# Kernel tuning notes

Measured on AMD Instinct MI355X. Metric: run time of the kernel, lower is better.

The kernel has to match this reference:

```python
import jax, jax.numpy as jnp
import numpy as np

N = 50000   # nodes
E = 800000  # edges
H = 4       # num_heads
D = 32      # out_dim
IN = 256    # in_dim


def setup_inputs() -> dict:
    key = jax.random.key(0)
    k0, k1, k2, k3, k4, k5 = jax.random.split(key, 6)
    h = jax.random.normal(k0, (N, IN), dtype=jnp.float32)
    # fl weight (torch Linear stores [out, in]), xavier-ish scale
    Wl = jax.random.normal(k1, (H * D, IN), dtype=jnp.float32) * (1.0 / np.sqrt(IN))
    # fc / fq are initialized to small constants in torch; use small random here
    fc = jax.random.normal(k2, (IN, H * D), dtype=jnp.float32) * 0.02
    fq = jax.random.normal(k3, (IN, H * D), dtype=jnp.float32) * 0.02
    src = jax.random.randint(k4, (E,), 0, N)
    dst = jax.random.randint(k5, (E,), 0, N)
    return {"h": h, "Wl": Wl, "fc": fc, "fq": fq, "src": src, "dst": dst}


def reference(h, Wl, fc, fq, src, dst):
    n = h.shape[0]
    ft = (h @ Wl.T).reshape(n, H, D)      # [N,H,D]
    ft_c = (h @ fc).reshape(n, H, D)      # [N,H,D]
    ft_q = (h @ fq).reshape(n, H, D)      # [N,H,D]

    # edge attention: c = ft_c[dst], q = ft_q[src] - c, a = ELU(sum(q*c))
    c = ft_c[dst]                         # [E,H,D]
    a = jax.nn.elu(jnp.sum((ft_q[src] - c) * c, axis=-1))  # [E,H]

    # segmented (per-destination) softmax over incoming edges, per head
    m = jax.ops.segment_max(a, dst, num_segments=n)        # [N,H]
    ex = jnp.exp(a - m[dst])
    s = jax.ops.segment_sum(ex, dst, num_segments=n)       # [N,H]
    attn = ex / s[dst]                                     # [E,H]

    # global top-k (smallest l_s) threshold + mass redistribution, per head
    l_s = int(0.713 * attn.shape[0])
    srt = jnp.sort(attn, axis=0)                           # ascending per head
    thd = srt[l_s - 1]                                     # [H] l_s-th smallest
    topk_sum = jnp.sum(srt[:l_s], axis=0)                  # [H]
    a2 = jnp.where(attn - thd < 0, jnp.zeros((), attn.dtype), attn)
    ratio = (jnp.sum(a2, axis=0) + topk_sum) / jnp.sum(a2, axis=0)  # [H]
    a3 = a2 * ratio                                        # [E,H]

    # weighted scatter-sum of source features to destinations
    out = jax.ops.segment_sum(ft[src] * a3[:, :, None], dst, num_segments=n)  # [N,H,D]

    # concat=True: cat(flattened heads, mean over heads of ft)
    return jnp.concatenate([out.reshape(n, -1), ft.mean(axis=1)], axis=1)  # [N, H*D + D]
```

## Files before the change

### kernel.cpp

```cpp
#include <hip/hip_runtime.h>
#include <hip/hip_bf16.h>
#include <math.h>

#define N_NODES 50000
#define N_EDGES 800000
#define DH 32
#define IN_DIM 256
#define OUTC 160
#define LS 570400
#define RANK0 (LS - 1)
#define DEG_CAP 160
#define BCAP 65536
#define MARG 3.0e-4

typedef unsigned long long u64;
#define SC_FX 1099511627776.0
#define SC_32 4294967296.0

__global__ void k_deg(const int* __restrict__ dst, unsigned* __restrict__ A){
  int e = blockIdx.x * 256 + threadIdx.x;
  if (e < N_EDGES) atomicAdd(&A[dst[e]], 1u);
}

__global__ __launch_bounds__(1024) void k_scan(unsigned* __restrict__ A){
  __shared__ unsigned ps[1024];
  int t = threadIdx.x;
  const int CH = (N_NODES + 1023) / 1024;
  int base = t * CH;
  unsigned s = 0;
  for (int i = 0; i < CH; i++){ int n = base + i; if (n < N_NODES) s += A[n]; }
  ps[t] = s;
  __syncthreads();
  for (int off = 1; off < 1024; off <<= 1){
    unsigned v = (t >= off) ? ps[t - off] : 0;
    __syncthreads();
    ps[t] += v;
    __syncthreads();
  }
  unsigned ex = (t == 0) ? 0 : ps[t - 1];
  for (int i = 0; i < CH; i++){
    int n = base + i;
    if (n < N_NODES){ unsigned dv = A[n]; A[n] = ex; ex += dv; }
  }
}

__global__ void k_fill(const int* __restrict__ dst, unsigned* __restrict__ A,
                       unsigned* __restrict__ eidx){
  int e = blockIdx.x * 256 + threadIdx.x;
  if (e < N_EDGES) eidx[atomicAdd(&A[dst[e]], 1u)] = (unsigned)e;
}

__global__ void k_init(unsigned* __restrict__ sel32, unsigned* __restrict__ krem,
                       unsigned* __restrict__ cnt, unsigned* __restrict__ done,
                       unsigned* __restrict__ ccnt, unsigned* __restrict__ cbelow,
                       unsigned* __restrict__ bcnt, unsigned* __restrict__ cntless,
                       u64* __restrict__ gsums){
  int t = threadIdx.x;
  if (t < 4){ sel32[t]=0; krem[t]=RANK0; cnt[t]=0; ccnt[t]=0; cbelow[t]=0; cntless[t]=0; }
  if (t < 8) gsums[t] = 0;
  if (t == 0){ done[0] = 0; bcnt[0] = 0; }
}

__global__ void k_prept(const float* __restrict__ fc, const float* __restrict__ fq,
                        float* __restrict__ fcT, float* __restrict__ fqT){
  int i = blockIdx.x * 256 + threadIdx.x;
  if (i >= IN_DIM * 128) return;
  int k = i >> 7, c = i & 127;
  fcT[(size_t)c * 256 + k] = fc[i];
  fqT[(size_t)c * 256 + k] = fq[i];
}

#define BM 128
#define BK 16
__global__ __launch_bounds__(256) void k_gemm384(const float* __restrict__ A,
    const float* __restrict__ Wl, const float* __restrict__ fc,
    const float* __restrict__ fq, float* __restrict__ C){
  __shared__ float As[BK][BM + 4];
  __shared__ float Bs[BK][128 + 4];
  int tid = threadIdx.x;
  int m0 = blockIdx.x * BM;
  int n0 = blockIdx.y * 128;
  int ty = tid / 16, tx = tid % 16;
  const float* Bsrc = (n0 == 128) ? fc : fq;

  int sA0r = (tid * 2) >> 2,     sA0c = (tid * 2) & 3;
  int sA1r = (tid * 2 + 1) >> 2, sA1c = (tid * 2 + 1) & 3;
  int sW0j = sA0r, sW0c = sA0c;
  int sW1j = sA1r, sW1c = sA1c;
  int sB0k = (tid * 2) >> 5,     sB0c = (tid * 2) & 31;
  int sB1k = (tid * 2 + 1) >> 5, sB1c = (tid * 2 + 1) & 31;

  float acc[8][8];
  #pragma unroll
  for (int i = 0; i < 8; i++)
    #pragma unroll
    for (int j = 0; j < 8; j++) acc[i][j] = 0.f;

  float4 rA0, rA1, rB0, rB1;
  {
    int r0 = m0 + sA0r, r1 = m0 + sA1r;
    rA0 = (r0 < N_NODES) ? *(const float4*)&A[(size_t)r0 * IN_DIM + sA0c * 4] : make_float4(0,0,0,0);
    rA1 = (r1 < N_NODES) ? *(const float4*)&A[(size_t)r1 * IN_DIM + sA1c * 4] : make_float4(0,0,0,0);
    if (n0 == 0){
      rB0 = *(const float4*)&Wl[(size_t)sW0j * IN_DIM + sW0c * 4];
      rB1 = *(const float4*)&Wl[(size_t)sW1j * IN_DIM + sW1c * 4];
    } else {
      rB0 = *(const float4*)&Bsrc[(size_t)sB0k * 128 + sB0c * 4];
      rB1 = *(const float4*)&Bsrc[(size_t)sB1k * 128 + sB1c * 4];
    }
  }

  for (int k0 = 0; k0 < IN_DIM; k0 += BK){
    As[sA0c * 4 + 0][sA0r] = rA0.x; As[sA0c * 4 + 1][sA0r] = rA0.y;
    As[sA0c * 4 + 2][sA0r] = rA0.z; As[sA0c * 4 + 3][sA0r] = rA0.w;
    As[sA1c * 4 + 0][sA1r] = rA1.x; As[sA1c * 4 + 1][sA1r] = rA1.y;
    As[sA1c * 4 + 2][sA1r] = rA1.z; As[sA1c * 4 + 3][sA1r] = rA1.w;
    if (n0 == 0){
      Bs[sW0c * 4 + 0][sW0j] = rB0.x; Bs[sW0c * 4 + 1][sW0j] = rB0.y;
      Bs[sW0c * 4 + 2][sW0j] = rB0.z; Bs[sW0c * 4 + 3][sW0j] = rB0.w;
      Bs[sW1c * 4 + 0][sW1j] = rB1.x; Bs[sW1c * 4 + 1][sW1j] = rB1.y;
      Bs[sW1c * 4 + 2][sW1j] = rB1.z; Bs[sW1c * 4 + 3][sW1j] = rB1.w;
    } else {
      *(float4*)&Bs[sB0k][sB0c * 4] = rB0;
      *(float4*)&Bs[sB1k][sB1c * 4] = rB1;
    }
    __syncthreads();
    if (k0 + BK < IN_DIM){
      int kn = k0 + BK;
      int r0 = m0 + sA0r, r1 = m0 + sA1r;
      rA0 = (r0 < N_NODES) ? *(const float4*)&A[(size_t)r0 * IN_DIM + kn + sA0c * 4] : make_float4(0,0,0,0);
      rA1 = (r1 < N_NODES) ? *(const float4*)&A[(size_t)r1 * IN_DIM + kn + sA1c * 4] : make_float4(0,0,0,0);
      if (n0 == 0){
        rB0 = *(const float4*)&Wl[(size_t)sW0j * IN_DIM + kn + sW0c * 4];
        rB1 = *(const float4*)&Wl[(size_t)sW1j * IN_DIM + kn + sW1c * 4];
      } else {
        rB0 = *(const float4*)&Bsrc[(size_t)(kn + sB0k) * 128 + sB0c * 4];
        rB1 = *(const float4*)&Bsrc[(size_t)(kn + sB1k) * 128 + sB1c * 4];
      }
    }
    #pragma unroll
    for (int kk = 0; kk < BK; kk++){
      float4 a0 = *(const float4*)&As[kk][ty * 4];
      float4 a1 = *(const float4*)&As[kk][64 + ty * 4];
      float4 b0 = *(const float4*)&Bs[kk][tx * 4];
      float4 b1 = *(const float4*)&Bs[kk][64 + tx * 4];
      float av[8] = {a0.x, a0.y, a0.z, a0.w, a1.x, a1.y, a1.z, a1.w};
      float bv[8] = {b0.x, b0.y, b0.z, b0.w, b1.x, b1.y, b1.z, b1.w};
      #pragma unroll
      for (int i = 0; i < 8; i++)
        #pragma unroll
        for (int j = 0; j < 8; j++)
          acc[i][j] = fmaf(av[i], bv[j], acc[i][j]);
    }
    __syncthreads();
  }
  #pragma unroll
  for (int i = 0; i < 8; i++){
    int r = m0 + ((i < 4) ? (ty * 4 + i) : (64 + ty * 4 + (i - 4)));
    if (r >= N_NODES) continue;
    *(float4*)&C[(size_t)r * 384 + n0 + tx * 4]      = make_float4(acc[i][0], acc[i][1], acc[i][2], acc[i][3]);
    *(float4*)&C[(size_t)r * 384 + n0 + 64 + tx * 4] = make_float4(acc[i][4], acc[i][5], acc[i][6], acc[i][7]);
  }
}

__global__ __launch_bounds__(256) void k_softedge32(const float* __restrict__ fcq,
    const int* __restrict__ src, const unsigned* __restrict__ A,
    const unsigned* __restrict__ eidx, float* __restrict__ abuf){
  __shared__ float lds_a[8][DEG_CAP * 4];
  int tid = threadIdx.x;
  int wv = tid >> 6;
  int l = tid & 63;
  int half = l >> 5;
  int ll = l & 31;
  int ds = wv * 2 + half;
  int d = blockIdx.x * 8 + ds;
  bool ok = (d < N_NODES);
  unsigned k0 = 0, k1 = 0;
  if (ok){ k0 = d ? A[d - 1] : 0u; k1 = A[d]; }
  unsigned deg = k1 - k0;
  float4 c4 = make_float4(0.f, 0.f, 0.f, 0.f);
  float4 q4n = make_float4(0.f, 0.f, 0.f, 0.f);
  if (deg){
    c4 = *(const float4*)&fcq[(size_t)d * 384 + 128 + ll * 4];
    int sn = src[eidx[k0]];
    q4n = *(const float4*)&fcq[(size_t)sn * 384 + 256 + ll * 4];
  }
  float m = -1.0e30f;
  for (unsigned kk = 0; kk < deg; kk++){
    float4 q4 = q4n;
    if (kk + 1 < deg){
      int s2 = src[eidx[k0 + kk + 1]];
      q4n = *(const float4*)&fcq[(size_t)s2 * 384 + 256 + ll * 4];
    }
    float v = (q4.x - c4.x) * c4.x;
    v = fmaf(q4.y - c4.y, c4.y, v);
    v = fmaf(q4.z - c4.z, c4.z, v);
    v = fmaf(q4.w - c4.w, c4.w, v);
    v += __shfl_xor(v, 1);
    v += __shfl_xor(v, 2);
    v += __shfl_xor(v, 4);
    float a = (v > 0.f) ? v : expm1f(v);
    m = fmaxf(m, a);
    if ((ll & 7) == 0) lds_a[ds][kk * 4 + (ll >> 3)] = a;
  }
  float mm = __shfl(m, half * 32 + (ll & 3) * 8);
  unsigned nj = deg * 4;
  long long sfx = 0;
  for (unsigned jj = ll; jj < nj; jj += 32){
    float ex = __expf(lds_a[ds][jj] - mm);
    lds_a[ds][jj] = ex;
    sfx += (long long)llrintf(ex * (float)SC_32);
  }
  sfx += __shfl_xor(sfx, 4);
  sfx += __shfl_xor(sfx, 8);
  sfx += __shfl_xor(sfx, 16);
  if (deg){
    float sd = (float)((double)sfx * (1.0 / SC_32));
    for (unsigned jj = ll; jj < nj; jj += 32)
      abuf[(size_t)k0 * 4 + jj] = lds_a[ds][jj] / sd;
  }
}

__global__ __launch_bounds__(256) void k_hp32(const float* __restrict__ attn,
    unsigned* __restrict__ sel32, unsigned* __restrict__ krem, unsigned* __restrict__ cnt,
    unsigned* __restrict__ hist, unsigned* __restrict__ done, unsigned maskHi, int shift){
  __shared__ unsigned lh[1024];
  __shared__ unsigned ticket;
  for (int j = threadIdx.x; j < 1024; j += 256) lh[j] = 0;
  __syncthreads();
  int i0 = blockIdx.x * 256 + threadIdx.x;
  int hh = i0 & 3;
  unsigned sel = sel32[hh] & maskHi;
  const int total = N_EDGES * 4;
  for (int i = i0; i < total; i += gridDim.x * 256){
    unsigned u = __float_as_uint(attn[i]);
    if ((u & maskHi) == sel)
      atomicAdd(&lh[hh * 256 + ((u >> shift) & 255u)], 1u);
  }
  __syncthreads();
  for (int j = threadIdx.x; j < 1024; j += 256)
    if (lh[j]) atomicAdd(&hist[j], lh[j]);
  __threadfence();
  if (threadIdx.x == 0) ticket = atomicAdd(done, 1u);
  __syncthreads();
  if (ticket == gridDim.x - 1){
    __threadfence();
    for (int j = threadIdx.x; j < 1024; j += 256){ lh[j] = hist[j]; hist[j] = 0; }
    __syncthreads();
    if (threadIdx.x < 4){
      int t = threadIdx.x;
      unsigned kr = krem[t], cum = 0, b = 0;
      for (; b < 256; b++){
        unsigned c2 = lh[t * 256 + b];
        if (kr < cum + c2) break;
        cum += c2;
      }
      sel32[t] |= b << shift;
      krem[t] = kr - cum;
      cnt[t] += cum;
    }
    if (threadIdx.x == 0) *done = 0;
  }
}

__global__ __launch_bounds__(256) void k_compact32(const float* __restrict__ attn,
    const unsigned* __restrict__ sel32, unsigned* __restrict__ ccnt,
    float* __restrict__ cand){
  __shared__ unsigned lcnt[4];
  __shared__ unsigned lbase[4];
  int t = threadIdx.x;
  if (t < 4) lcnt[t] = 0;
  __syncthreads();
  int i0 = blockIdx.x * 256 + t;
  int hh = i0 & 3;
  unsigned sel = sel32[hh] & 0xFFFF0000u;
  const int total = N_EDGES * 4;
  unsigned mc = 0;
  for (int i = i0; i < total; i += gridDim.x * 256){
    unsigned u = __float_as_uint(attn[i]);
    if ((u & 0xFFFF0000u) == sel) mc++;
  }
  unsigned my_local = mc ? atomicAdd(&lcnt[hh], mc) : 0u;
  __syncthreads();
  if (t < 4) lbase[t] = lcnt[t] ? atomicAdd(&ccnt[t], lcnt[t]) : 0u;
  __syncthreads();
  if (mc == 0) return;
  unsigned pos = lbase[hh] + my_local;
  float* cp = cand + (size_t)hh * N_EDGES;
  for (int i = i0; i < total; i += gridDim.x * 256){
    float v = attn[i];
    unsigned u = __float_as_uint(v);
    if ((u & 0xFFFF0000u) == sel) cp[pos++] = v;
  }
}

__global__ __launch_bounds__(256) void k_fin32(const float* __restrict__ cand,
    const unsigned* __restrict__ ccnt, unsigned* __restrict__ sel32,
    unsigned* __restrict__ krem, unsigned* __restrict__ cnt,
    unsigned* __restrict__ hist, unsigned* __restrict__ done, int shift){
  __shared__ unsigned lh[256];
  __shared__ unsigned ticket;
  int t = threadIdx.x;
  lh[t] = 0;
  __syncthreads();
  int h = blockIdx.x & 3;
  int bidx = blockIdx.x >> 2;
  int bph = gridDim.x >> 2;
  unsigned maskHi = ~((1u << (shift + 8)) - 1u);
  unsigned sel = sel32[h] & maskHi;
  unsigned n = ccnt[h];
  const float* cp = cand + (size_t)h * N_EDGES;
  for (unsigned i = bidx * 256 + t; i < n; i += bph * 256){
    unsigned u = __float_as_uint(cp[i]);
    if ((u & maskHi) == sel) atomicAdd(&lh[(u >> shift) & 255u], 1u);
  }
  __syncthreads();
  if (lh[t]) atomicAdd(&hist[h * 256 + t], lh[t]);
  __threadfence();
  if (t == 0) ticket = atomicAdd(done, 1u);
  __syncthreads();
  if (ticket == gridDim.x - 1){
    __threadfence();
    __shared__ unsigned fh[1024];
    for (int j = t; j < 1024; j += 256){ fh[j] = hist[j]; hist[j] = 0; }
    __syncthreads();
    if (t < 4){
      unsigned kr = krem[t], cum = 0, b = 0;
      for (; b < 256; b++){
        unsigned c2 = fh[t * 256 + b];
        if (kr < cum + c2) break;
        cum += c2;
      }
      sel32[t] |= b << shift;
      krem[t] = kr - cum;
      cnt[t] += cum;
    }
    if (t == 0) *done = 0;
  }
}

__global__ __launch_bounds__(256) void k_bmark(const float* __restrict__ attn,
    const unsigned* __restrict__ sel32, unsigned* __restrict__ cbelow,
    unsigned* __restrict__ bcnt, unsigned* __restrict__ blist){
  int t = threadIdx.x;
  int i0 = blockIdx.x * 256 + t;
  int hh = t & 3;
  double thd = (double)__uint_as_float(sel32[hh]);
  double lo = thd * (1.0 - MARG), hi = thd * (1.0 + MARG);
  unsigned below = 0;
  const int total = N_EDGES * 4;
  for (int i = i0; i < total; i += gridDim.x * 256){
    double v = (double)attn[i];
    if (v < lo) below++;
    else if (v <= hi){
      unsigned p = atomicAdd(bcnt, 1u);
      if (p < BCAP) blist[p] = (unsigned)i;
    }
  }
  #pragma unroll
  for (int m = 4; m < 64; m <<= 1) below += __shfl_xor(below, m);
  __shared__ unsigned sb[16];
  int wv = t >> 6;
  if ((t & 63) < 4) sb[wv * 4 + hh] = below;
  __syncthreads();
  if (t < 4){
    unsigned b = sb[t] + sb[4 + t] + sb[8 + t] + sb[12 + t];
    if (b) atomicAdd(&cbelow[t], b);
  }
}

__global__ __launch_bounds__(256) void k_brefine(const float* __restrict__ h,
    const float* __restrict__ fcT, const float* __restrict__ fqT,
    const int* __restrict__ src, const int* __restrict__ dst,
    const unsigned* __restrict__ A, const unsigned* __restrict__ eidx,
    const unsigned* __restrict__ blist, const unsigned* __restrict__ bcnt,
    double* __restrict__ bval){
  __shared__ float wqs[32][257];
  __shared__ double cs[32];
  __shared__ double la[DEG_CAP];
  int tid = threadIdx.x;
  int wv = tid >> 6;
  int l = tid & 63;
  int j = l & 31;
  int khalf = l >> 5;
  unsigned nb = *bcnt; if (nb > BCAP) nb = BCAP;
  for (unsigned idx = blockIdx.x; idx < nb; idx += gridDim.x){
    unsigned slot = blist[idx];
    unsigned kslot = slot >> 2;
    int hh = slot & 3;
    int d = dst[eidx[kslot]];
    unsigned k0 = d ? A[d - 1] : 0u, k1 = A[d];
    unsigned deg = k1 - k0;
    {
      int col = tid >> 3, seg = tid & 7;
      const float* gsrc = fqT + (size_t)(hh * 32 + col) * 256 + seg * 32;
      #pragma unroll
      for (int r = 0; r < 8; r++){
        float4 v = *(const float4*)&gsrc[r * 4];
        float* wdst = &wqs[col][seg * 32 + r * 4];
        wdst[0] = v.x; wdst[1] = v.y; wdst[2] = v.z; wdst[3] = v.w;
      }
    }
    __syncthreads();
    if (wv == 0){
      const float* hd = h + (size_t)d * 256 + khalf * 128;
      const float* wc = fcT + (size_t)(hh * 32 + j) * 256 + khalf * 128;
      double c0 = 0.0, c1 = 0.0, c2 = 0.0, c3 = 0.0;
      #pragma unroll 8
      for (int i = 0; i < 128; i += 4){
        float4 hv = *(const float4*)&hd[i];
        float4 w2 = *(const float4*)&wc[i];
        c0 = fma((double)hv.x, (double)w2.x, c0);
        c1 = fma((double)hv.y, (double)w2.y, c1);
        c2 = fma((double)hv.z, (double)w2.z, c2);
        c3 = fma((double)hv.w, (double)w2.w, c3);
      }
      double c = (c0 + c1) + (c2 + c3);
      c += __shfl_xor(c, 32);
      if (l < 32) cs[l] = c;
    }
    __syncthreads();
    double cj = cs[j];
    for (unsigned k = k0 + wv; k < k1; k += 4){
      int s = src[eidx[k]];
      const float* hs = h + (size_t)s * 256 + khalf * 128;
      const float* wr = &wqs[j][khalf * 128];
      float4 hv = *(const float4*)&hs[0];
      double q0 = 0.0, q1 = 0.0, q2 = 0.0, q3 = 0.0;
      #pragma unroll 4
      for (int i = 0; i < 128; i += 4){
        float4 cur = hv;
        if (i + 4 < 128) hv = *(const float4*)&hs[i + 4];
        q0 = fma((double)cur.x, (double)wr[i + 0], q0);
        q1 = fma((double)cur.y, (double)wr[i + 1], q1);
        q2 = fma((double)cur.z, (double)wr[i + 2], q2);
        q3 = fma((double)cur.w, (double)wr[i + 3], q3);
      }
      double q = (q0 + q1) + (q2 + q3);
      q += __shfl_xor(q, 32);
      double p = (q - cj) * cj;
      p += __shfl_xor(p, 1);
      p += __shfl_xor(p, 2);
      p += __shfl_xor(p, 4);
      p += __shfl_xor(p, 8);
      p += __shfl_xor(p, 16);
      double a = (p > 0.0) ? p : expm1(p);
      if (l == 0) la[k - k0] = a;
    }
    __syncthreads();
    if (wv == 0){
      double m = -1.0e300;
      for (unsigned kk = l; kk < deg; kk += 64) m = fmax(m, la[kk]);
      #pragma unroll
      for (int msk = 1; msk < 64; msk <<= 1) m = fmax(m, __shfl_xor(m, msk));
      long long sfx = 0;
      for (unsigned kk = l; kk < deg; kk += 64)
        sfx += llrint(exp(la[kk] - m) * SC_FX);
      #pragma unroll
      for (int msk = 1; msk < 64; msk <<= 1) sfx += __shfl_xor(sfx, msk);
      if (l == 0){
        double sd = (double)sfx * (1.0 / SC_FX);
        bval[idx] = exp(la[kslot - k0] - m) / sd;
      }
    }
    __syncthreads();
  }
}

__global__ __launch_bounds__(256) void k_bselect(const double* __restrict__ bval,
    const unsigned* __restrict__ blist, const unsigned* __restrict__ bcnt,
    const unsigned* __restrict__ cbelow, double* __restrict__ thd64,
    unsigned* __restrict__ cntless){
  __shared__ unsigned lh[256];
  __shared__ u64 s_sel;
  __shared__ unsigned s_kr, s_cnt;
  int hsel = blockIdx.x;
  int t = threadIdx.x;
  unsigned nb = *bcnt; if (nb > BCAP) nb = BCAP;
  if (t == 0){ s_sel = 0; s_kr = RANK0 - cbelow[hsel]; s_cnt = 0; }
  __syncthreads();
  for (int p = 0; p < 8; p++){
    int shift = 56 - 8 * p;
    u64 maskHi = (p == 0) ? 0ull : (~0ull) << (64 - 8 * p);
    lh[t] = 0;
    __syncthreads();
    u64 sel = s_sel;
    for (unsigned i = t; i < nb; i += 256){
      if ((int)(blist[i] & 3) == hsel){
        u64 u = (u64)__double_as_longlong(bval[i]);
        if ((u & maskHi) == sel) atomicAdd(&lh[(unsigned)((u >> shift) & 255u)], 1u);
      }
    }
    __syncthreads();
    if (t == 0){
      unsigned kr = s_kr, cum = 0, b = 0;
      for (; b < 256; b++){
        unsigned c2 = lh[b];
        if (kr < cum + c2) break;
        cum += c2;
      }
      s_sel |= ((u64)b) << shift;
      s_kr = kr - cum;
      s_cnt += cum;
    }
    __syncthreads();
  }
  if (t == 0){
    thd64[hsel] = __longlong_as_double((long long)s_sel);
    cntless[hsel] = cbelow[hsel] + s_cnt;
  }
}

__global__ __launch_bounds__(256) void k_sums32(const float* __restrict__ attn,
    const unsigned* __restrict__ sel32, u64* __restrict__ gsums, float* __restrict__ a3){
  int t = threadIdx.x;
  int i0 = blockIdx.x * 256 + t;
  int hh = t & 3;
  double thd = (double)__uint_as_float(sel32[hh]);
  double lo = thd * (1.0 - MARG), hi = thd * (1.0 + MARG);
  double al = 0.0, ag = 0.0;
  const int total = N_EDGES * 4;
  for (int i = i0; i < total; i += gridDim.x * 256){
    float vf = attn[i];
    double v = (double)vf;
    if (v < lo){ al += v; a3[i] = 0.f; }
    else if (v > hi){ ag += v; a3[i] = vf; }
    else a3[i] = 0.f;
  }
  long long ql = llrint(al * SC_FX);
  long long qg = llrint(ag * SC_FX);
  #pragma unroll
  for (int m = 4; m < 64; m <<= 1){
    ql += __shfl_xor(ql, m);
    qg += __shfl_xor(qg, m);
  }
  __shared__ long long sl[16], sg[16];
  int wv = t >> 6;
  if ((t & 63) < 4){ sl[wv * 4 + hh] = ql; sg[wv * 4 + hh] = qg; }
  __syncthreads();
  if (t < 4){
    long long a = sl[t] + sl[4 + t] + sl[8 + t] + sl[12 + t];
    long long b = sg[t] + sg[4 + t] + sg[8 + t] + sg[12 + t];
    if (a) atomicAdd(&gsums[t],     (u64)a);
    if (b) atomicAdd(&gsums[4 + t], (u64)b);
  }
}

__global__ void k_bfinal(const unsigned* __restrict__ blist, const double* __restrict__ bval,
    const unsigned* __restrict__ bcnt, const double* __restrict__ thd64,
    u64* __restrict__ gsums, float* __restrict__ a3){
  unsigned nb = *bcnt; if (nb > BCAP) nb = BCAP;
  for (unsigned idx = blockIdx.x * 256 + threadIdx.x; idx < nb; idx += gridDim.x * 256){
    unsigned slot = blist[idx];
    int hh = slot & 3;
    double v = bval[idx];
    bool kept = (v >= thd64[hh]);
    a3[slot] = kept ? (float)v : 0.f;
    atomicAdd(&gsums[(kept ? 4 : 0) + hh], (u64)llrint(v * SC_FX));
  }
}

__global__ void k_ratio(const double* __restrict__ thd64, const unsigned* __restrict__ cntless,
                        const u64* __restrict__ gsums, double* __restrict__ trd){
  int t = threadIdx.x;
  if (t < 4){
    double sless = (double)(long long)gsums[t]     * (1.0 / SC_FX);
    double sge   = (double)(long long)gsums[4 + t] * (1.0 / SC_FX);
    double topk  = sless + (double)(LS - (int)cntless[t]) * thd64[t];
    trd[t] = thd64[t];
    trd[4 + t] = (sge + topk) / sge;
  }
}

__global__ __launch_bounds__(256) void k_scatter2(const float* __restrict__ fcq,
    const int* __restrict__ src, const unsigned* __restrict__ A,
    const unsigned* __restrict__ eidx, const float* __restrict__ a3,
    const double* __restrict__ trd, float* __restrict__ out){
  int d = blockIdx.x * 4 + (threadIdx.x >> 6);
  int t = threadIdx.x & 63;
  if (d >= N_NODES) return;
  int hh = t >> 4;
  double ratio = trd[4 + hh];
  unsigned k0 = d ? A[d - 1] : 0u, k1 = A[d];
  long long acc0 = 0, acc1 = 0;
  float wn = (k0 < k1) ? a3[(size_t)k0 * 4 + hh] : 0.f;
  unsigned en = (k0 < k1) ? eidx[k0] : 0u;
  for (unsigned k = k0; k < k1; k++){
    float w = wn;
    unsigned e = en;
    if (k + 1 < k1){ wn = a3[(size_t)(k + 1) * 4 + hh]; en = eidx[k + 1]; }
    if (__ballot(w != 0.f) == 0ull) continue;
    if (w != 0.f){
      int s = src[e];
      float2 f = *(const float2*)&fcq[(size_t)s * 384 + t * 2];
      double a3r = (double)w * ratio;
      acc0 += llrint(a3r * (double)f.x * SC_FX);
      acc1 += llrint(a3r * (double)f.y * SC_FX);
    }
  }
  float* p = &out[(size_t)d * OUTC + t * 2];
  p[0] = (float)((double)acc0 * (1.0 / SC_FX));
  p[1] = (float)((double)acc1 * (1.0 / SC_FX));
}

__global__ void k_mean(const float* __restrict__ fcq, float* __restrict__ out){
  int i = blockIdx.x * 256 + threadIdx.x;
  if (i >= N_NODES * DH) return;
  int n = i / DH, dd = i % DH;
  const float* p = fcq + (size_t)n * 384;
  out[(size_t)n * OUTC + 128 + dd] = 0.25f * (p[dd] + p[32 + dd] + p[64 + dd] + p[96 + dd]);
}

extern "C" void kernel_launch(void* const* d_in, const int* in_sizes, int n_in,
                              void* d_out, int out_size, void* d_ws, size_t ws_size,
                              hipStream_t stream){
  const float* h  = (const float*)d_in[0];
  const float* Wl = (const float*)d_in[1];
  const float* fc = (const float*)d_in[2];
  const float* fq = (const float*)d_in[3];
  const int* src  = (const int*)d_in[4];
  const int* dst  = (const int*)d_in[5];
  float* out = (float*)d_out;

  char* ws = (char*)d_ws;
  float*    fcq  = (float*)(ws);
  unsigned* A    = (unsigned*)(ws + 76800000);
  unsigned* eidx = (unsigned*)(ws + 77000064);
  float*    a3   = (float*)(ws + 80200064);
  unsigned* hist = (unsigned*)(ws + 93000064);
  unsigned* sel32  = (unsigned*)(ws + 93004160);
  unsigned* krem   = (unsigned*)(ws + 93004176);
  unsigned* cnt    = (unsigned*)(ws + 93004192);
  unsigned* done   = (unsigned*)(ws + 93004208);
  unsigned* ccnt   = (unsigned*)(ws + 93004224);
  unsigned* cbelow = (unsigned*)(ws + 93004240);
  unsigned* bcnt   = (unsigned*)(ws + 93004256);
  unsigned* cntless= (unsigned*)(ws + 93004272);
  u64*      gsums  = (u64*)(ws + 93004288);
  double*   thd64  = (double*)(ws + 93004352);
  double*   trd    = (double*)(ws + 93004416);
  unsigned* blist  = (unsigned*)(ws + 93008896);
  double*   bval   = (double*)(ws + 93271040);
  float*    fcT    = (float*)(ws + 93795328);
  float*    fqT    = (float*)(ws + 93926400);

  float* abuf = (float*)d_out;
  float* cand = (float*)((char*)d_out + 12800000);

  hipMemsetAsync(A, 0, 200004, stream);
  hipMemsetAsync(hist, 0, 4096, stream);
  k_init<<<1, 64, 0, stream>>>(sel32, krem, cnt, done, ccnt, cbelow, bcnt, cntless, gsums);
  k_prept<<<(IN_DIM * 128 + 255) / 256, 256, 0, stream>>>(fc, fq, fcT, fqT);

  k_deg<<<(N_EDGES + 255) / 256, 256, 0, stream>>>(dst, A);
  k_scan<<<1, 1024, 0, stream>>>(A);
  k_fill<<<(N_EDGES + 255) / 256, 256, 0, stream>>>(dst, A, eidx);

  dim3 gg((N_NODES + BM - 1) / BM, 3);
  k_gemm384<<<gg, 256, 0, stream>>>(h, Wl, fc, fq, fcq);

  k_softedge32<<<(N_NODES + 7) / 8, 256, 0, stream>>>(fcq, src, A, eidx, abuf);

  k_hp32<<<1024, 256, 0, stream>>>(abuf, sel32, krem, cnt, hist, done, 0u, 24);
  k_hp32<<<1024, 256, 0, stream>>>(abuf, sel32, krem, cnt, hist, done, 0xFF000000u, 16);
  k_compact32<<<1024, 256, 0, stream>>>(abuf, sel32, ccnt, cand);
  k_fin32<<<256, 256, 0, stream>>>(cand, ccnt, sel32, krem, cnt, hist, done, 8);
  k_fin32<<<256, 256, 0, stream>>>(cand, ccnt, sel32, krem, cnt, hist, done, 0);

  k_bmark<<<1024, 256, 0, stream>>>(abuf, sel32, cbelow, bcnt, blist);
  k_brefine<<<2048, 256, 0, stream>>>(h, fcT, fqT, src, dst, A, eidx, blist, bcnt, bval);
  k_bselect<<<4, 256, 0, stream>>>(bval, blist, bcnt, cbelow, thd64, cntless);

  k_sums32<<<2048, 256, 0, stream>>>(abuf, sel32, gsums, a3);
  k_bfinal<<<64, 256, 0, stream>>>(blist, bval, bcnt, thd64, gsums, a3);
  k_ratio<<<1, 64, 0, stream>>>(thd64, cntless, gsums, trd);

  k_scatter2<<<(N_NODES + 3) / 4, 256, 0, stream>>>(fcq, src, A, eidx, a3, trd, out);
  k_mean<<<(N_NODES * DH + 255) / 256, 256, 0, stream>>>(fcq, out);
}
```

Baseline: 965.7 us.

## Fuse band marking with threshold sums, fold head-mean into scatter, double-buffer GEMM

The band-marking pass and the threshold partial-sum pass are merged into one kernel, so the 3.2M attention values are read once instead of twice and one launch is dropped. The per-node head-mean is computed inside the scatter kernel, which removes the separate k_mean launch and its extra pass over fcq. The GEMM now uses double-buffered shared-memory tiles so one __syncthreads per k-step is dropped, at the cost of twice the LDS footprint. All three are launch and memory-traffic reductions on a chain of many small kernels.

New measurement: 934.9 us. 3.2% less time.

```diff
diff --git a/kernel.cpp b/kernel.cpp
--- a/kernel.cpp
+++ b/kernel.cpp
@@ -75,8 +75,8 @@
 __global__ __launch_bounds__(256) void k_gemm384(const float* __restrict__ A,
     const float* __restrict__ Wl, const float* __restrict__ fc,
     const float* __restrict__ fq, float* __restrict__ C){
-  __shared__ float As[BK][BM + 4];
-  __shared__ float Bs[BK][128 + 4];
+  __shared__ float As[2][BK][BM + 4];
+  __shared__ float Bs[2][BK][128 + 4];
   int tid = threadIdx.x;
   int m0 = blockIdx.x * BM;
   int n0 = blockIdx.y * 128;
@@ -85,8 +85,6 @@
 
   int sA0r = (tid * 2) >> 2,     sA0c = (tid * 2) & 3;
   int sA1r = (tid * 2 + 1) >> 2, sA1c = (tid * 2 + 1) & 3;
-  int sW0j = sA0r, sW0c = sA0c;
-  int sW1j = sA1r, sW1c = sA1c;
   int sB0k = (tid * 2) >> 5,     sB0c = (tid * 2) & 31;
   int sB1k = (tid * 2 + 1) >> 5, sB1c = (tid * 2 + 1) & 31;
 
@@ -102,27 +100,28 @@
     rA0 = (r0 < N_NODES) ? *(const float4*)&A[(size_t)r0 * IN_DIM + sA0c * 4] : make_float4(0,0,0,0);
     rA1 = (r1 < N_NODES) ? *(const float4*)&A[(size_t)r1 * IN_DIM + sA1c * 4] : make_float4(0,0,0,0);
     if (n0 == 0){
-      rB0 = *(const float4*)&Wl[(size_t)sW0j * IN_DIM + sW0c * 4];
-      rB1 = *(const float4*)&Wl[(size_t)sW1j * IN_DIM + sW1c * 4];
+      rB0 = *(const float4*)&Wl[(size_t)sA0r * IN_DIM + sA0c * 4];
+      rB1 = *(const float4*)&Wl[(size_t)sA1r * IN_DIM + sA1c * 4];
     } else {
       rB0 = *(const float4*)&Bsrc[(size_t)sB0k * 128 + sB0c * 4];
       rB1 = *(const float4*)&Bsrc[(size_t)sB1k * 128 + sB1c * 4];
     }
   }
 
+  int p = 0;
   for (int k0 = 0; k0 < IN_DIM; k0 += BK){
-    As[sA0c * 4 + 0][sA0r] = rA0.x; As[sA0c * 4 + 1][sA0r] = rA0.y;
-    As[sA0c * 4 + 2][sA0r] = rA0.z; As[sA0c * 4 + 3][sA0r] = rA0.w;
-    As[sA1c * 4 + 0][sA1r] = rA1.x; As[sA1c * 4 + 1][sA1r] = rA1.y;
-    As[sA1c * 4 + 2][sA1r] = rA1.z; As[sA1c * 4 + 3][sA1r] = rA1.w;
+    As[p][sA0c * 4 + 0][sA0r] = rA0.x; As[p][sA0c * 4 + 1][sA0r] = rA0.y;
+    As[p][sA0c * 4 + 2][sA0r] = rA0.z; As[p][sA0c * 4 + 3][sA0r] = rA0.w;
+    As[p][sA1c * 4 + 0][sA1r] = rA1.x; As[p][sA1c * 4 + 1][sA1r] = rA1.y;
+    As[p][sA1c * 4 + 2][sA1r] = rA1.z; As[p][sA1c * 4 + 3][sA1r] = rA1.w;
     if (n0 == 0){
-      Bs[sW0c * 4 + 0][sW0j] = rB0.x; Bs[sW0c * 4 + 1][sW0j] = rB0.y;
-      Bs[sW0c * 4 + 2][sW0j] = rB0.z; Bs[sW0c * 4 + 3][sW0j] = rB0.w;
-      Bs[sW1c * 4 + 0][sW1j] = rB1.x; Bs[sW1c * 4 + 1][sW1j] = rB1.y;
-      Bs[sW1c * 4 + 2][sW1j] = rB1.z; Bs[sW1c * 4 + 3][sW1j] = rB1.w;
+      Bs[p][sA0c * 4 + 0][sA0r] = rB0.x; Bs[p][sA0c * 4 + 1][sA0r] = rB0.y;
+      Bs[p][sA0c * 4 + 2][sA0r] = rB0.z; Bs[p][sA0c * 4 + 3][sA0r] = rB0.w;
+      Bs[p][sA1c * 4 + 0][sA1r] = rB1.x; Bs[p][sA1c * 4 + 1][sA1r] = rB1.y;
+      Bs[p][sA1c * 4 + 2][sA1r] = rB1.z; Bs[p][sA1c * 4 + 3][sA1r] = rB1.w;
     } else {
-      *(float4*)&Bs[sB0k][sB0c * 4] = rB0;
-      *(float4*)&Bs[sB1k][sB1c * 4] = rB1;
+      *(float4*)&Bs[p][sB0k][sB0c * 4] = rB0;
+      *(float4*)&Bs[p][sB1k][sB1c * 4] = rB1;
     }
     __syncthreads();
     if (k0 + BK < IN_DIM){
@@ -131,8 +130,8 @@
       rA0 = (r0 < N_NODES) ? *(const float4*)&A[(size_t)r0 * IN_DIM + kn + sA0c * 4] : make_float4(0,0,0,0);
       rA1 = (r1 < N_NODES) ? *(const float4*)&A[(size_t)r1 * IN_DIM + kn + sA1c * 4] : make_float4(0,0,0,0);
       if (n0 == 0){
-        rB0 = *(const float4*)&Wl[(size_t)sW0j * IN_DIM + kn + sW0c * 4];
-        rB1 = *(const float4*)&Wl[(size_t)sW1j * IN_DIM + kn + sW1c * 4];
+        rB0 = *(const float4*)&Wl[(size_t)sA0r * IN_DIM + kn + sA0c * 4];
+        rB1 = *(const float4*)&Wl[(size_t)sA1r * IN_DIM + kn + sA1c * 4];
       } else {
         rB0 = *(const float4*)&Bsrc[(size_t)(kn + sB0k) * 128 + sB0c * 4];
         rB1 = *(const float4*)&Bsrc[(size_t)(kn + sB1k) * 128 + sB1c * 4];
@@ -140,10 +139,10 @@
     }
     #pragma unroll
     for (int kk = 0; kk < BK; kk++){
-      float4 a0 = *(const float4*)&As[kk][ty * 4];
-      float4 a1 = *(const float4*)&As[kk][64 + ty * 4];
-      float4 b0 = *(const float4*)&Bs[kk][tx * 4];
-      float4 b1 = *(const float4*)&Bs[kk][64 + tx * 4];
+      float4 a0 = *(const float4*)&As[p][kk][ty * 4];
+      float4 a1 = *(const float4*)&As[p][kk][64 + ty * 4];
+      float4 b0 = *(const float4*)&Bs[p][kk][tx * 4];
+      float4 b1 = *(const float4*)&Bs[p][kk][64 + tx * 4];
       float av[8] = {a0.x, a0.y, a0.z, a0.w, a1.x, a1.y, a1.z, a1.w};
       float bv[8] = {b0.x, b0.y, b0.z, b0.w, b1.x, b1.y, b1.z, b1.w};
       #pragma unroll
@@ -152,7 +151,7 @@
         for (int j = 0; j < 8; j++)
           acc[i][j] = fmaf(av[i], bv[j], acc[i][j]);
     }
-    __syncthreads();
+    p ^= 1;
   }
   #pragma unroll
   for (int i = 0; i < 8; i++){
@@ -339,33 +338,49 @@
   }
 }
 
-__global__ __launch_bounds__(256) void k_bmark(const float* __restrict__ attn,
+__global__ __launch_bounds__(256) void k_marksums(const float* __restrict__ attn,
     const unsigned* __restrict__ sel32, unsigned* __restrict__ cbelow,
-    unsigned* __restrict__ bcnt, unsigned* __restrict__ blist){
+    unsigned* __restrict__ bcnt, unsigned* __restrict__ blist,
+    u64* __restrict__ gsums, float* __restrict__ a3){
   int t = threadIdx.x;
   int i0 = blockIdx.x * 256 + t;
   int hh = t & 3;
   double thd = (double)__uint_as_float(sel32[hh]);
   double lo = thd * (1.0 - MARG), hi = thd * (1.0 + MARG);
+  double al = 0.0, ag = 0.0;
   unsigned below = 0;
   const int total = N_EDGES * 4;
   for (int i = i0; i < total; i += gridDim.x * 256){
-    double v = (double)attn[i];
-    if (v < lo) below++;
-    else if (v <= hi){
+    float vf = attn[i];
+    double v = (double)vf;
+    if (v < lo){ al += v; below++; a3[i] = 0.f; }
+    else if (v > hi){ ag += v; a3[i] = vf; }
+    else {
       unsigned p = atomicAdd(bcnt, 1u);
       if (p < BCAP) blist[p] = (unsigned)i;
-    }
-  }
+      a3[i] = 0.f;
+    }
+  }
+  long long ql = llrint(al * SC_FX);
+  long long qg = llrint(ag * SC_FX);
   #pragma unroll
-  for (int m = 4; m < 64; m <<= 1) below += __shfl_xor(below, m);
+  for (int m = 4; m < 64; m <<= 1){
+    ql += __shfl_xor(ql, m);
+    qg += __shfl_xor(qg, m);
+    below += __shfl_xor(below, m);
+  }
+  __shared__ long long sl[16], sg[16];
   __shared__ unsigned sb[16];
   int wv = t >> 6;
-  if ((t & 63) < 4) sb[wv * 4 + hh] = below;
+  if ((t & 63) < 4){ sl[wv * 4 + hh] = ql; sg[wv * 4 + hh] = qg; sb[wv * 4 + hh] = below; }
   __syncthreads();
   if (t < 4){
-    unsigned b = sb[t] + sb[4 + t] + sb[8 + t] + sb[12 + t];
-    if (b) atomicAdd(&cbelow[t], b);
+    long long a = sl[t] + sl[4 + t] + sl[8 + t] + sl[12 + t];
+    long long b = sg[t] + sg[4 + t] + sg[8 + t] + sg[12 + t];
+    unsigned bl = sb[t] + sb[4 + t] + sb[8 + t] + sb[12 + t];
+    if (a) atomicAdd(&gsums[t],     (u64)a);
+    if (b) atomicAdd(&gsums[4 + t], (u64)b);
+    if (bl) atomicAdd(&cbelow[t], bl);
   }
 }
 
@@ -511,41 +526,6 @@
   }
 }
 
-__global__ __launch_bounds__(256) void k_sums32(const float* __restrict__ attn,
-    const unsigned* __restrict__ sel32, u64* __restrict__ gsums, float* __restrict__ a3){
-  int t = threadIdx.x;
-  int i0 = blockIdx.x * 256 + t;
-  int hh = t & 3;
-  double thd = (double)__uint_as_float(sel32[hh]);
-  double lo = thd * (1.0 - MARG), hi = thd * (1.0 + MARG);
-  double al = 0.0, ag = 0.0;
-  const int total = N_EDGES * 4;
-  for (int i = i0; i < total; i += gridDim.x * 256){
-    float vf = attn[i];
-    double v = (double)vf;
-    if (v < lo){ al += v; a3[i] = 0.f; }
-    else if (v > hi){ ag += v; a3[i] = vf; }
-    else a3[i] = 0.f;
-  }
-  long long ql = llrint(al * SC_FX);
-  long long qg = llrint(ag * SC_FX);
-  #pragma unroll
-  for (int m = 4; m < 64; m <<= 1){
-    ql += __shfl_xor(ql, m);
-    qg += __shfl_xor(qg, m);
-  }
-  __shared__ long long sl[16], sg[16];
-  int wv = t >> 6;
-  if ((t & 63) < 4){ sl[wv * 4 + hh] = ql; sg[wv * 4 + hh] = qg; }
-  __syncthreads();
-  if (t < 4){
-    long long a = sl[t] + sl[4 + t] + sl[8 + t] + sl[12 + t];
-    long long b = sg[t] + sg[4 + t] + sg[8 + t] + sg[12 + t];
-    if (a) atomicAdd(&gsums[t],     (u64)a);
-    if (b) atomicAdd(&gsums[4 + t], (u64)b);
-  }
-}
-
 __global__ void k_bfinal(const unsigned* __restrict__ blist, const double* __restrict__ bval,
     const unsigned* __restrict__ bcnt, const double* __restrict__ thd64,
     u64* __restrict__ gsums, float* __restrict__ a3){
@@ -601,14 +581,10 @@
   float* p = &out[(size_t)d * OUTC + t * 2];
   p[0] = (float)((double)acc0 * (1.0 / SC_FX));
   p[1] = (float)((double)acc1 * (1.0 / SC_FX));
-}
-
-__global__ void k_mean(const float* __restrict__ fcq, float* __restrict__ out){
-  int i = blockIdx.x * 256 + threadIdx.x;
-  if (i >= N_NODES * DH) return;
-  int n = i / DH, dd = i % DH;
-  const float* p = fcq + (size_t)n * 384;
-  out[(size_t)n * OUTC + 128 + dd] = 0.25f * (p[dd] + p[32 + dd] + p[64 + dd] + p[96 + dd]);
+  if (t < 32){
+    const float* pf = &fcq[(size_t)d * 384];
+    out[(size_t)d * OUTC + 128 + t] = 0.25f * (pf[t] + pf[32 + t] + pf[64 + t] + pf[96 + t]);
+  }
 }
 
 extern "C" void kernel_launch(void* const* d_in, const int* in_sizes, int n_in,
@@ -667,14 +643,12 @@
   k_fin32<<<256, 256, 0, stream>>>(cand, ccnt, sel32, krem, cnt, hist, done, 8);
   k_fin32<<<256, 256, 0, stream>>>(cand, ccnt, sel32, krem, cnt, hist, done, 0);
 
-  k_bmark<<<1024, 256, 0, stream>>>(abuf, sel32, cbelow, bcnt, blist);
+  k_marksums<<<2048, 256, 0, stream>>>(abuf, sel32, cbelow, bcnt, blist, gsums, a3);
+
   k_brefine<<<2048, 256, 0, stream>>>(h, fcT, fqT, src, dst, A, eidx, blist, bcnt, bval);
   k_bselect<<<4, 256, 0, stream>>>(bval, blist, bcnt, cbelow, thd64, cntless);
-
-  k_sums32<<<2048, 256, 0, stream>>>(abuf, sel32, gsums, a3);
   k_bfinal<<<64, 256, 0, stream>>>(blist, bval, bcnt, thd64, gsums, a3);
   k_ratio<<<1, 64, 0, stream>>>(thd64, cntless, gsums, trd);
 
   k_scatter2<<<(N_NODES + 3) / 4, 256, 0, stream>>>(fcq, src, A, eidx, a3, trd, out);
-  k_mean<<<(N_NODES * DH + 255) / 256, 256, 0, stream>>>(fcq, out);
-}
+}
```
